# Kernel tuning notes

Measured on AMD Instinct MI355X. Metric: run time of the kernel, lower is better.

## Reference

```python
import jax, jax.numpy as jnp
import numpy as np

T, B, C = 2048, 8, 1024
H, K, P = 16, 31, 15  # num_heads, kernel_size, padding_l
R = C // H


def setup_inputs() -> dict:
    key = jax.random.key(0)
    k1, k2 = jax.random.split(key)
    x = jax.random.normal(k1, (T, B, C), dtype=jnp.float32)
    # weight_linear.weight, xavier-ish scale, shape (H*K, C)
    W = jax.random.normal(k2, (H * K, C), dtype=jnp.float32) * (2.0 / (C + H * K)) ** 0.5
    return {"x": x, "W": W}


def reference(x, W):
    # per-position dynamic kernels: (T,B,H,K)
    w = jnp.einsum('tbc,oc->tbo', x, W).reshape(T, B, H, K)
    w = jax.nn.softmax(w, axis=-1)  # weight_softmax=True
    # depthwise dynamic conv: out[t] = sum_k w[t,:,:,k] * x[t - P + k]
    xr = x.reshape(T, B, H, R)
    xp = jnp.pad(xr, ((P, K - 1 - P), (0, 0), (0, 0), (0, 0)))
    out = jnp.zeros_like(xr)
    for k in range(K):  # fixed small kernel-size loop, fuses under jit
        out = out + w[:, :, :, k:k + 1] * jax.lax.dynamic_slice_in_dim(xp, k, T, axis=0)
    return out.reshape(T, B, C)
```

## Files before the change

kernel.cpp:

```cpp
#include <hip/hip_runtime.h>
#include <cstddef>
#include <cstdint>

constexpr int T_ = 2048;
constexpr int B_ = 8;
constexpr int C_ = 1024;
constexpr int H_ = 16;
constexpr int K_ = 31;
constexpr int P_ = 15;
constexpr int M_ = T_ * B_;
constexpr int N_ = H_ * K_;
constexpr int NP = 512;

typedef _Float16 f16x4 __attribute__((ext_vector_type(4)));
typedef _Float16 f16x8 __attribute__((ext_vector_type(8)));
typedef float f32x4 __attribute__((ext_vector_type(4)));

__device__ __forceinline__ void async_cp16(const void* g, void* l) {
    __builtin_amdgcn_global_load_lds(
        (const __attribute__((address_space(1))) void*)g,
        (__attribute__((address_space(3))) void*)l, 16, 0, 0);
}

constexpr int XCH = M_ * C_ / 8;
constexpr int WCH = NP * C_ / 8;

__global__ __launch_bounds__(256)
void cvt_inputs(const float* __restrict__ X, const float* __restrict__ W,
                _Float16* __restrict__ Xh, _Float16* __restrict__ Wh) {
    const int id = blockIdx.x * 256 + threadIdx.x;
    if (id < XCH) {
        const float4 v0 = *(const float4*)(X + (size_t)id * 8);
        const float4 v1 = *(const float4*)(X + (size_t)id * 8 + 4);
        f16x8 hv;
        hv[0] = (_Float16)v0.x; hv[1] = (_Float16)v0.y;
        hv[2] = (_Float16)v0.z; hv[3] = (_Float16)v0.w;
        hv[4] = (_Float16)v1.x; hv[5] = (_Float16)v1.y;
        hv[6] = (_Float16)v1.z; hv[7] = (_Float16)v1.w;
        *(f16x8*)(Xh + (size_t)id * 8) = hv;
    } else {
        const int j = id - XCH;
        const int n = j >> 7, sp = j & 127;
        const int h = n >> 5, k = n & 31;
        f16x8 hv = {};
        if (k < 31) {
            const float* wp = W + (size_t)(h * 31 + k) * C_ + sp * 8;
            const float4 v0 = *(const float4*)(wp);
            const float4 v1 = *(const float4*)(wp + 4);
            hv[0] = (_Float16)v0.x; hv[1] = (_Float16)v0.y;
            hv[2] = (_Float16)v0.z; hv[3] = (_Float16)v0.w;
            hv[4] = (_Float16)v1.x; hv[5] = (_Float16)v1.y;
            hv[6] = (_Float16)v1.z; hv[7] = (_Float16)v1.w;
        }
        *(f16x8*)(Wh + (size_t)n * C_ + sp * 8) = hv;
    }
}

__global__ __launch_bounds__(256)
void gemm_logits(const _Float16* __restrict__ Xh,
                 const _Float16* __restrict__ Wh,
                 _Float16* __restrict__ Lg) {
    __shared__ _Float16 As[3][128 * 64];
    __shared__ _Float16 Bs[2][128 * 64];

    const int tid = threadIdx.x;
    const int lane = tid & 63;
    const int w = tid >> 6;
    const int wm = (w >> 1) * 64;
    const int wn = (w & 1) * 64;
    const int col = lane & 15;
    const int g = lane >> 4;

    const int id = (int)blockIdx.x;
    const int bx = (id & 7) | ((id >> 5) << 3);
    const int by = (id >> 3) & 3;
    const int m0 = bx * 128;
    const int n0 = by * 128;

    const _Float16* asrc[4];
    const _Float16* bsrc[4];
#pragma unroll
    for (int p = 0; p < 4; ++p) {
        const int ci = p * 256 + tid;
        const int r = ci >> 3, cs = ci & 7;
        const int cl = cs ^ (r & 7);
        asrc[p] = Xh + (size_t)(m0 + r) * C_ + cl * 8;
        bsrc[p] = Wh + (size_t)(n0 + r) * C_ + cl * 8;
    }

    f32x4 acc[4][4] = {};

#pragma unroll
    for (int p = 0; p < 4; ++p) {
        const int ci = p * 256 + tid;
        async_cp16(asrc[p], &As[0][ci * 8]);
    }
#pragma unroll
    for (int p = 0; p < 4; ++p) {
        const int ci = p * 256 + tid;
        async_cp16(bsrc[p], &Bs[0][ci * 8]);
    }
#pragma unroll
    for (int p = 0; p < 4; ++p) {
        const int ci = p * 256 + tid;
        async_cp16(asrc[p] + 64, &As[1][ci * 8]);
    }
    asm volatile("s_waitcnt vmcnt(4)" ::: "memory");
    __builtin_amdgcn_s_barrier();
    __builtin_amdgcn_sched_barrier(0);

    for (int t = 0; t < 16; ++t) {
        const int ca = t % 3, cb = t & 1;
        if (t < 15) {
            const int k1 = (t + 1) * 64;
#pragma unroll
            for (int p = 0; p < 4; ++p) {
                const int ci = p * 256 + tid;
                async_cp16(bsrc[p] + k1, &Bs[cb ^ 1][ci * 8]);
            }
        }
        if (t < 14) {
            const int k2 = (t + 2) * 64;
            const int ca2 = (t + 2) % 3;
#pragma unroll
            for (int p = 0; p < 4; ++p) {
                const int ci = p * 256 + tid;
                async_cp16(asrc[p] + k2, &As[ca2][ci * 8]);
            }
        }

        f16x8 a[2][4], b[2][4];
#pragma unroll
        for (int kk = 0; kk < 2; ++kk) {
#pragma unroll
            for (int mf = 0; mf < 4; ++mf) {
                const int row = wm + mf * 16 + col;
                const int c = ((kk << 2) | g) ^ (row & 7);
                a[kk][mf] = *(const f16x8*)&As[ca][row * 64 + c * 8];
            }
#pragma unroll
            for (int nf = 0; nf < 4; ++nf) {
                const int row = wn + nf * 16 + col;
                const int c = ((kk << 2) | g) ^ (row & 7);
                b[kk][nf] = *(const f16x8*)&Bs[cb][row * 64 + c * 8];
            }
        }
#pragma unroll
        for (int kk = 0; kk < 2; ++kk)
#pragma unroll
            for (int nf = 0; nf < 4; ++nf)
#pragma unroll
                for (int mf = 0; mf < 4; ++mf)
                    acc[mf][nf] = __builtin_amdgcn_mfma_f32_16x16x32_f16(
                        a[kk][mf], b[kk][nf], acc[kk ? mf : mf][nf], 0, 0, 0);

        if (t < 14) {
            asm volatile("s_waitcnt vmcnt(4)" ::: "memory");
        } else {
            asm volatile("s_waitcnt vmcnt(0)" ::: "memory");
        }
        __builtin_amdgcn_s_barrier();
        __builtin_amdgcn_sched_barrier(0);
    }

    const int rb = g * 4;
#pragma unroll
    for (int nf = 0; nf < 4; ++nf) {
        const int nl = wn + nf * 16 + col;
#pragma unroll
        for (int mf = 0; mf < 4; ++mf) {
            const int row = wm + mf * 16 + rb;
#pragma unroll
            for (int r = 0; r < 4; ++r)
                Lg[(size_t)(m0 + row + r) * NP + n0 + nl] =
                    (_Float16)acc[mf][nf][r];
        }
    }
}

__global__ __launch_bounds__(256)
void dconv(const _Float16* __restrict__ Xh, const _Float16* __restrict__ Lg,
           float* __restrict__ out) {
    __shared__ float xs[94][64];
    __shared__ _Float16 ws16[64][40];

    const int tid = threadIdx.x;
    const int t0 = blockIdx.x * 64;
    const int bh = (int)blockIdx.y;
    const int b = bh >> 4, h = bh & 15;

    for (int task = tid; task < 94 * 8; task += 256) {
        const int r = task >> 3, hc = task & 7;
        const int tp = t0 + r - 15;
        f16x8 v = {};
        if (tp >= 0 && tp < T_)
            v = *(const f16x8*)(Xh + ((size_t)tp * B_ + b) * C_ + h * 64 + hc * 8);
        f32x4 lo, hi;
        lo[0] = (float)v[0]; lo[1] = (float)v[1];
        lo[2] = (float)v[2]; lo[3] = (float)v[3];
        hi[0] = (float)v[4]; hi[1] = (float)v[5];
        hi[2] = (float)v[6]; hi[3] = (float)v[7];
        const int c0 = (2 * hc) ^ (r & 7), c1 = (2 * hc + 1) ^ (r & 7);
        *(f32x4*)&xs[r][c0 * 4] = lo;
        *(f32x4*)&xs[r][c1 * 4] = hi;
    }
    {
        const int t = tid >> 2, kc = (tid & 3) * 8;
        const f16x8 wv =
            *(const f16x8*)(Lg + ((size_t)(t0 + t) * B_ + b) * NP + h * 32 + kc);
        *(f16x8*)&ws16[t][kc] = wv;
    }
    __syncthreads();

    if (tid < 64) {
        float v[31];
        float mx = -1e30f;
#pragma unroll
        for (int k = 0; k < 31; ++k) {
            v[k] = (float)ws16[tid][k];
            mx = fmaxf(mx, v[k]);
        }
        float ssum = 0.f;
#pragma unroll
        for (int k = 0; k < 31; ++k) { v[k] = __expf(v[k] - mx); ssum += v[k]; }
        const float inv = 1.f / ssum;
#pragma unroll
        for (int k = 0; k < 31; ++k) ws16[tid][k] = (_Float16)(v[k] * inv);
    }
    __syncthreads();

    const int s = tid & 15;
    const int tg4 = (tid >> 4) * 4;
    f32x4 acc[4] = {};
    f32x4 wc[4];

#pragma unroll
    for (int rr = 0; rr < 34; ++rr) {
        const int r = tg4 + rr;
        const f32x4 xv = *(const f32x4*)&xs[r][(s ^ (r & 7)) * 4];
#pragma unroll
        for (int i = 0; i < 4; ++i) {
            const int k = rr - i;
            if (k < 0 || k > 30) continue;
            if ((k & 3) == 0) {
                const f16x4 wq = *(const f16x4*)&ws16[tg4 + i][k];
                wc[i][0] = (float)wq[0]; wc[i][1] = (float)wq[1];
                wc[i][2] = (float)wq[2]; wc[i][3] = (float)wq[3];
            }
            acc[i] += wc[i][k & 3] * xv;
        }
    }

#pragma unroll
    for (int i = 0; i < 4; ++i) {
        const int t = t0 + tg4 + i;
        *(f32x4*)(out + ((size_t)t * B_ + b) * C_ + h * 64 + s * 4) = acc[i];
    }
}

extern "C" void kernel_launch(void* const* d_in, const int* in_sizes, int n_in,
                              void* d_out, int out_size, void* d_ws,
                              size_t ws_size, hipStream_t stream) {
    const float* X = (const float*)d_in[0];
    const float* W = (const float*)d_in[1];
    float* out = (float*)d_out;

    _Float16* Wh = (_Float16*)d_ws;
    _Float16* Lg = (_Float16*)((char*)d_ws + (size_t)NP * C_ * 2);
    _Float16* Xh = (_Float16*)((char*)d_ws + (size_t)NP * C_ * 2 +
                               (size_t)M_ * NP * 2);

    cvt_inputs<<<(XCH + WCH) / 256, 256, 0, stream>>>(X, W, Xh, Wh);
    gemm_logits<<<512, 256, 0, stream>>>(Xh, Wh, Lg);
    dconv<<<dim3(T_ / 64, B_ * H_), 256, 0, stream>>>(Xh, Lg, out);
}
```

Measured before the change: 70.15 us.

## Drop the separate X fp16 conversion pass; convert fp32 X inside the GEMM loads

Removes the pre-pass that converted all of X to fp16. The GEMM now streams fp32 X tiles into LDS through async copies and converts them to fp16 when building the MFMA fragments. The depthwise conv reads fp32 X directly. This cuts a full read-and-write pass over the large activation, but doubles A-tile bytes and LDS use in the GEMM (about 128KB per block), which likely allows fewer resident blocks per CU.

```diff
diff --git a/kernel.cpp b/kernel.cpp
--- a/kernel.cpp
+++ b/kernel.cpp
@@ -22,45 +22,28 @@
         (__attribute__((address_space(3))) void*)l, 16, 0, 0);
 }
 
-constexpr int XCH = M_ * C_ / 8;
-constexpr int WCH = NP * C_ / 8;
-
 __global__ __launch_bounds__(256)
-void cvt_inputs(const float* __restrict__ X, const float* __restrict__ W,
-                _Float16* __restrict__ Xh, _Float16* __restrict__ Wh) {
-    const int id = blockIdx.x * 256 + threadIdx.x;
-    if (id < XCH) {
-        const float4 v0 = *(const float4*)(X + (size_t)id * 8);
-        const float4 v1 = *(const float4*)(X + (size_t)id * 8 + 4);
-        f16x8 hv;
+void cvt_w(const float* __restrict__ W, _Float16* __restrict__ Wh) {
+    const int j = blockIdx.x * 256 + threadIdx.x;
+    const int n = j >> 7, sp = j & 127;
+    const int h = n >> 5, k = n & 31;
+    f16x8 hv = {};
+    if (k < 31) {
+        const float* wp = W + (size_t)(h * 31 + k) * C_ + sp * 8;
+        const float4 v0 = *(const float4*)(wp);
+        const float4 v1 = *(const float4*)(wp + 4);
         hv[0] = (_Float16)v0.x; hv[1] = (_Float16)v0.y;
         hv[2] = (_Float16)v0.z; hv[3] = (_Float16)v0.w;
         hv[4] = (_Float16)v1.x; hv[5] = (_Float16)v1.y;
         hv[6] = (_Float16)v1.z; hv[7] = (_Float16)v1.w;
-        *(f16x8*)(Xh + (size_t)id * 8) = hv;
-    } else {
-        const int j = id - XCH;
-        const int n = j >> 7, sp = j & 127;
-        const int h = n >> 5, k = n & 31;
-        f16x8 hv = {};
-        if (k < 31) {
-            const float* wp = W + (size_t)(h * 31 + k) * C_ + sp * 8;
-            const float4 v0 = *(const float4*)(wp);
-            const float4 v1 = *(const float4*)(wp + 4);
-            hv[0] = (_Float16)v0.x; hv[1] = (_Float16)v0.y;
-            hv[2] = (_Float16)v0.z; hv[3] = (_Float16)v0.w;
-            hv[4] = (_Float16)v1.x; hv[5] = (_Float16)v1.y;
-            hv[6] = (_Float16)v1.z; hv[7] = (_Float16)v1.w;
-        }
-        *(f16x8*)(Wh + (size_t)n * C_ + sp * 8) = hv;
-    }
+    }
+    *(f16x8*)(Wh + (size_t)n * C_ + sp * 8) = hv;
 }
 
 __global__ __launch_bounds__(256)
-void gemm_logits(const _Float16* __restrict__ Xh,
-                 const _Float16* __restrict__ Wh,
+void gemm_logits(const float* __restrict__ X, const _Float16* __restrict__ Wh,
                  _Float16* __restrict__ Lg) {
-    __shared__ _Float16 As[3][128 * 64];
+    __shared__ float As[3][128 * 64];
     __shared__ _Float16 Bs[2][128 * 64];
 
     const int tid = threadIdx.x;
@@ -77,57 +60,49 @@
     const int m0 = bx * 128;
     const int n0 = by * 128;
 
-    const _Float16* asrc[4];
+    const float* asrc[8];
+#pragma unroll
+    for (int p = 0; p < 8; ++p) {
+        const int ci = p * 256 + tid;
+        const int r = ci >> 4, cs = ci & 15;
+        const int cl = (cs & 8) | ((cs ^ r) & 7);
+        asrc[p] = X + (size_t)(m0 + r) * C_ + cl * 4;
+    }
     const _Float16* bsrc[4];
 #pragma unroll
     for (int p = 0; p < 4; ++p) {
         const int ci = p * 256 + tid;
         const int r = ci >> 3, cs = ci & 7;
         const int cl = cs ^ (r & 7);
-        asrc[p] = Xh + (size_t)(m0 + r) * C_ + cl * 8;
         bsrc[p] = Wh + (size_t)(n0 + r) * C_ + cl * 8;
     }
 
     f32x4 acc[4][4] = {};
 
-#pragma unroll
-    for (int p = 0; p < 4; ++p) {
-        const int ci = p * 256 + tid;
-        async_cp16(asrc[p], &As[0][ci * 8]);
-    }
-#pragma unroll
-    for (int p = 0; p < 4; ++p) {
-        const int ci = p * 256 + tid;
-        async_cp16(bsrc[p], &Bs[0][ci * 8]);
-    }
-#pragma unroll
-    for (int p = 0; p < 4; ++p) {
-        const int ci = p * 256 + tid;
-        async_cp16(asrc[p] + 64, &As[1][ci * 8]);
-    }
-    asm volatile("s_waitcnt vmcnt(4)" ::: "memory");
+#define ISSUE_A(k0, buf)                                                  \
+    _Pragma("unroll")                                                     \
+    for (int p = 0; p < 8; ++p) {                                         \
+        const int ci = p * 256 + tid;                                     \
+        async_cp16(asrc[p] + (k0), &As[buf][ci * 4]);                     \
+    }
+#define ISSUE_B(k0, buf)                                                  \
+    _Pragma("unroll")                                                     \
+    for (int p = 0; p < 4; ++p) {                                         \
+        const int ci = p * 256 + tid;                                     \
+        async_cp16(bsrc[p] + (k0), &Bs[buf][ci * 8]);                     \
+    }
+
+    ISSUE_A(0, 0);
+    ISSUE_B(0, 0);
+    ISSUE_A(64, 1);
+    asm volatile("s_waitcnt vmcnt(8)" ::: "memory");
     __builtin_amdgcn_s_barrier();
     __builtin_amdgcn_sched_barrier(0);
 
     for (int t = 0; t < 16; ++t) {
         const int ca = t % 3, cb = t & 1;
-        if (t < 15) {
-            const int k1 = (t + 1) * 64;
-#pragma unroll
-            for (int p = 0; p < 4; ++p) {
-                const int ci = p * 256 + tid;
-                async_cp16(bsrc[p] + k1, &Bs[cb ^ 1][ci * 8]);
-            }
-        }
-        if (t < 14) {
-            const int k2 = (t + 2) * 64;
-            const int ca2 = (t + 2) % 3;
-#pragma unroll
-            for (int p = 0; p < 4; ++p) {
-                const int ci = p * 256 + tid;
-                async_cp16(asrc[p] + k2, &As[ca2][ci * 8]);
-            }
-        }
+        if (t < 15) { ISSUE_B((t + 1) * 64, cb ^ 1); }
+        if (t < 14) { ISSUE_A((t + 2) * 64, (t + 2) % 3); }
 
         f16x8 a[2][4], b[2][4];
 #pragma unroll
@@ -135,8 +110,17 @@
 #pragma unroll
             for (int mf = 0; mf < 4; ++mf) {
                 const int row = wm + mf * 16 + col;
-                const int c = ((kk << 2) | g) ^ (row & 7);
-                a[kk][mf] = *(const f16x8*)&As[ca][row * 64 + c * 8];
+                const int l0 = kk * 8 + 2 * g;
+                const int p0 = (l0 & 8) | ((l0 ^ row) & 7);
+                const int p1 = p0 ^ 1;
+                const f32x4 va = *(const f32x4*)&As[ca][row * 64 + p0 * 4];
+                const f32x4 vb = *(const f32x4*)&As[ca][row * 64 + p1 * 4];
+                f16x8 hv;
+                hv[0] = (_Float16)va[0]; hv[1] = (_Float16)va[1];
+                hv[2] = (_Float16)va[2]; hv[3] = (_Float16)va[3];
+                hv[4] = (_Float16)vb[0]; hv[5] = (_Float16)vb[1];
+                hv[6] = (_Float16)vb[2]; hv[7] = (_Float16)vb[3];
+                a[kk][mf] = hv;
             }
 #pragma unroll
             for (int nf = 0; nf < 4; ++nf) {
@@ -152,16 +136,18 @@
 #pragma unroll
                 for (int mf = 0; mf < 4; ++mf)
                     acc[mf][nf] = __builtin_amdgcn_mfma_f32_16x16x32_f16(
-                        a[kk][mf], b[kk][nf], acc[kk ? mf : mf][nf], 0, 0, 0);
+                        a[kk][mf], b[kk][nf], acc[mf][nf], 0, 0, 0);
 
         if (t < 14) {
-            asm volatile("s_waitcnt vmcnt(4)" ::: "memory");
+            asm volatile("s_waitcnt vmcnt(8)" ::: "memory");
         } else {
             asm volatile("s_waitcnt vmcnt(0)" ::: "memory");
         }
         __builtin_amdgcn_s_barrier();
         __builtin_amdgcn_sched_barrier(0);
     }
+#undef ISSUE_A
+#undef ISSUE_B
 
     const int rb = g * 4;
 #pragma unroll
@@ -179,7 +165,7 @@
 }
 
 __global__ __launch_bounds__(256)
-void dconv(const _Float16* __restrict__ Xh, const _Float16* __restrict__ Lg,
+void dconv(const float* __restrict__ X, const _Float16* __restrict__ Lg,
            float* __restrict__ out) {
     __shared__ float xs[94][64];
     __shared__ _Float16 ws16[64][40];
@@ -189,20 +175,13 @@
     const int bh = (int)blockIdx.y;
     const int b = bh >> 4, h = bh & 15;
 
-    for (int task = tid; task < 94 * 8; task += 256) {
-        const int r = task >> 3, hc = task & 7;
+    for (int task = tid; task < 94 * 16; task += 256) {
+        const int r = task >> 4, sc = task & 15;
         const int tp = t0 + r - 15;
-        f16x8 v = {};
+        f32x4 v = {};
         if (tp >= 0 && tp < T_)
-            v = *(const f16x8*)(Xh + ((size_t)tp * B_ + b) * C_ + h * 64 + hc * 8);
-        f32x4 lo, hi;
-        lo[0] = (float)v[0]; lo[1] = (float)v[1];
-        lo[2] = (float)v[2]; lo[3] = (float)v[3];
-        hi[0] = (float)v[4]; hi[1] = (float)v[5];
-        hi[2] = (float)v[6]; hi[3] = (float)v[7];
-        const int c0 = (2 * hc) ^ (r & 7), c1 = (2 * hc + 1) ^ (r & 7);
-        *(f32x4*)&xs[r][c0 * 4] = lo;
-        *(f32x4*)&xs[r][c1 * 4] = hi;
+            v = *(const f32x4*)(X + ((size_t)tp * B_ + b) * C_ + h * 64 + sc * 4);
+        *(f32x4*)&xs[r][(sc ^ (r & 7)) * 4] = v;
     }
     {
         const int t = tid >> 2, kc = (tid & 3) * 8;
@@ -267,10 +246,8 @@
 
     _Float16* Wh = (_Float16*)d_ws;
     _Float16* Lg = (_Float16*)((char*)d_ws + (size_t)NP * C_ * 2);
-    _Float16* Xh = (_Float16*)((char*)d_ws + (size_t)NP * C_ * 2 +
-                               (size_t)M_ * NP * 2);
-
-    cvt_inputs<<<(XCH + WCH) / 256, 256, 0, stream>>>(X, W, Xh, Wh);
-    gemm_logits<<<512, 256, 0, stream>>>(Xh, Wh, Lg);
-    dconv<<<dim3(T_ / 64, B_ * H_), 256, 0, stream>>>(Xh, Lg, out);
-}
+
+    cvt_w<<<256, 256, 0, stream>>>(W, Wh);
+    gemm_logits<<<512, 256, 0, stream>>>(X, Wh, Lg);
+    dconv<<<dim3(T_ / 64, B_ * H_), 256, 0, stream>>>(X, Lg, out);
+}
```

Result: slower. 94.71 us (+35.0%).

## Load GEMM B fragments directly from global memory, dropping the LDS staging buffer

Applied to the files above, without the earlier changes.

The logits GEMM no longer stages the W tile through shared memory. Each wave now reads its B fragments straight from global memory into registers at the start of every k-step, while the A tile keeps its triple-buffered async LDS pipeline. The waitcnt placement is reorganised, and launch bounds now request two blocks per CU. This cuts LDS traffic and footprint and removes the B async copies. The trade-off is that global/L2 load latency now sits inside each iteration with no prefetch, and waves sharing the same columns load the same W data twice.

```diff
diff --git a/kernel.cpp b/kernel.cpp
--- a/kernel.cpp
+++ b/kernel.cpp
@@ -56,12 +56,11 @@
     }
 }
 
-__global__ __launch_bounds__(256)
+__global__ __launch_bounds__(256, 2)
 void gemm_logits(const _Float16* __restrict__ Xh,
                  const _Float16* __restrict__ Wh,
                  _Float16* __restrict__ Lg) {
     __shared__ _Float16 As[3][128 * 64];
-    __shared__ _Float16 Bs[2][128 * 64];
 
     const int tid = threadIdx.x;
     const int lane = tid & 63;
@@ -78,73 +77,66 @@
     const int n0 = by * 128;
 
     const _Float16* asrc[4];
-    const _Float16* bsrc[4];
 #pragma unroll
     for (int p = 0; p < 4; ++p) {
         const int ci = p * 256 + tid;
         const int r = ci >> 3, cs = ci & 7;
         const int cl = cs ^ (r & 7);
         asrc[p] = Xh + (size_t)(m0 + r) * C_ + cl * 8;
-        bsrc[p] = Wh + (size_t)(n0 + r) * C_ + cl * 8;
+    }
+    const _Float16* bfrag[4];
+#pragma unroll
+    for (int nf = 0; nf < 4; ++nf) {
+        const int row = n0 + wn + nf * 16 + col;
+        bfrag[nf] = Wh + (size_t)row * C_ + g * 8;
     }
 
     f32x4 acc[4][4] = {};
 
-#pragma unroll
-    for (int p = 0; p < 4; ++p) {
-        const int ci = p * 256 + tid;
-        async_cp16(asrc[p], &As[0][ci * 8]);
-    }
-#pragma unroll
-    for (int p = 0; p < 4; ++p) {
-        const int ci = p * 256 + tid;
-        async_cp16(bsrc[p], &Bs[0][ci * 8]);
-    }
-#pragma unroll
-    for (int p = 0; p < 4; ++p) {
-        const int ci = p * 256 + tid;
-        async_cp16(asrc[p] + 64, &As[1][ci * 8]);
-    }
+#define ISSUE_A(k0, buf)                                                  \
+    _Pragma("unroll")                                                     \
+    for (int p = 0; p < 4; ++p) {                                         \
+        const int ci = p * 256 + tid;                                     \
+        async_cp16(asrc[p] + (k0), &As[buf][ci * 8]);                     \
+    }
+
+    ISSUE_A(0, 0);
+    ISSUE_A(64, 1);
     asm volatile("s_waitcnt vmcnt(4)" ::: "memory");
     __builtin_amdgcn_s_barrier();
     __builtin_amdgcn_sched_barrier(0);
 
     for (int t = 0; t < 16; ++t) {
-        const int ca = t % 3, cb = t & 1;
-        if (t < 15) {
-            const int k1 = (t + 1) * 64;
-#pragma unroll
-            for (int p = 0; p < 4; ++p) {
-                const int ci = p * 256 + tid;
-                async_cp16(bsrc[p] + k1, &Bs[cb ^ 1][ci * 8]);
-            }
-        }
-        if (t < 14) {
-            const int k2 = (t + 2) * 64;
-            const int ca2 = (t + 2) % 3;
-#pragma unroll
-            for (int p = 0; p < 4; ++p) {
-                const int ci = p * 256 + tid;
-                async_cp16(asrc[p] + k2, &As[ca2][ci * 8]);
-            }
-        }
-
-        f16x8 a[2][4], b[2][4];
-#pragma unroll
-        for (int kk = 0; kk < 2; ++kk) {
+        const int ca = t % 3;
+
+        f16x8 b[2][4];
+#pragma unroll
+        for (int kk = 0; kk < 2; ++kk)
+#pragma unroll
+            for (int nf = 0; nf < 4; ++nf)
+                b[kk][nf] = *(const f16x8*)(bfrag[nf] + t * 64 + kk * 32);
+        __builtin_amdgcn_sched_barrier(0);
+
+        if (t < 14) { ISSUE_A((t + 2) * 64, (t + 2) % 3); }
+        __builtin_amdgcn_sched_barrier(0);
+
+        f16x8 a[2][4];
+#pragma unroll
+        for (int kk = 0; kk < 2; ++kk)
 #pragma unroll
             for (int mf = 0; mf < 4; ++mf) {
                 const int row = wm + mf * 16 + col;
                 const int c = ((kk << 2) | g) ^ (row & 7);
                 a[kk][mf] = *(const f16x8*)&As[ca][row * 64 + c * 8];
             }
-#pragma unroll
-            for (int nf = 0; nf < 4; ++nf) {
-                const int row = wn + nf * 16 + col;
-                const int c = ((kk << 2) | g) ^ (row & 7);
-                b[kk][nf] = *(const f16x8*)&Bs[cb][row * 64 + c * 8];
-            }
-        }
+
+        if (t < 14) {
+            asm volatile("s_waitcnt vmcnt(4) lgkmcnt(0)" ::: "memory");
+        } else {
+            asm volatile("s_waitcnt vmcnt(0) lgkmcnt(0)" ::: "memory");
+        }
+        __builtin_amdgcn_sched_barrier(0);
+
 #pragma unroll
         for (int kk = 0; kk < 2; ++kk)
 #pragma unroll
@@ -152,16 +144,12 @@
 #pragma unroll
                 for (int mf = 0; mf < 4; ++mf)
                     acc[mf][nf] = __builtin_amdgcn_mfma_f32_16x16x32_f16(
-                        a[kk][mf], b[kk][nf], acc[kk ? mf : mf][nf], 0, 0, 0);
-
-        if (t < 14) {
-            asm volatile("s_waitcnt vmcnt(4)" ::: "memory");
-        } else {
-            asm volatile("s_waitcnt vmcnt(0)" ::: "memory");
-        }
+                        a[kk][mf], b[kk][nf], acc[mf][nf], 0, 0, 0);
+
         __builtin_amdgcn_s_barrier();
         __builtin_amdgcn_sched_barrier(0);
     }
+#undef ISSUE_A
 
     const int rb = g * 4;
 #pragma unroll
```

Result: slower. 84.84 us (+20.9%).
